# Performance work log

Hardware: AMD Instinct MI355X
Metric: run time of the kernel (lower is better)

Reference implementation:

```python
import jax, jax.numpy as jnp
import numpy as np

B, N, E, D = 8, 4096, 65536, 256


def setup_inputs() -> dict:
    key = jax.random.key(0)
    ks = jax.random.split(key, 4)
    return {
        "node_features": jax.random.normal(ks[0], (B, N, D), dtype=jnp.float32),
        "W": jax.random.normal(ks[1], (D, D), dtype=jnp.float32) * (1.0 / np.sqrt(D)),
        "b": jnp.zeros((D,), dtype=jnp.float32),
        "gamma": jnp.ones((D,), dtype=jnp.float32),
        "beta": jnp.zeros((D,), dtype=jnp.float32),
        "edge_index": jax.random.randint(ks[2], (B, 2, E), 0, N, dtype=jnp.int64),
        "node_mask": jax.random.randint(ks[3], (B, N), 0, 2, dtype=jnp.int32),
    }


def reference(node_features, W, b, gamma, beta, edge_index, node_mask):
    # Linear projection: h = x @ W^T + b   (nn.Linear convention, W: [out, in])
    h = jnp.einsum("bni,oi->bno", node_features, W) + b  # [B, N, D]
    batch, n_nodes, d = h.shape
    n_edges = edge_index.shape[2]

    src = edge_index[:, 0, :]  # [B, E]
    tgt = edge_index[:, 1, :]  # [B, E]

    nm = node_mask.astype(h.dtype)  # [B, N]
    # edge valid iff both endpoints are valid nodes
    emask = jnp.take_along_axis(nm, src, axis=1) * jnp.take_along_axis(nm, tgt, axis=1)  # [B, E]

    # gather source features, mask invalid edges
    msg = jnp.take_along_axis(h, src[..., None], axis=1) * emask[..., None]  # [B, E, D]

    # batched scatter-add via flat segment_sum with per-batch offsets
    seg_ids = (tgt + jnp.arange(batch, dtype=tgt.dtype)[:, None] * n_nodes).reshape(-1)
    agg = jax.ops.segment_sum(msg.reshape(batch * n_edges, d), seg_ids,
                              num_segments=batch * n_nodes).reshape(batch, n_nodes, d)

    h = h + agg / jnp.sqrt(jnp.asarray(n_nodes, h.dtype))

    # dropout is identity in eval mode
    # LayerNorm over last dim (eps = 1e-5, torch default)
    mu = jnp.mean(h, axis=-1, keepdims=True)
    var = jnp.mean((h - mu) ** 2, axis=-1, keepdims=True)
    h = (h - mu) * jax.lax.rsqrt(var + 1e-5) * gamma + beta

    h = jax.nn.relu(h)
    return h * nm[..., None]
```

## Files before the change

kernel.cpp:

```cpp
#include <hip/hip_runtime.h>
#include <hip/hip_bf16.h>

#define NN 4096
#define DIM 256
#define NE 65536
#define TOT_NODES 32768
#define TOT_EDGES 524288

__device__ __forceinline__ float ldf(const void* p, int isbf, size_t i) {
    return isbf ? __bfloat162float(((const __hip_bfloat16*)p)[i]) : ((const float*)p)[i];
}
__device__ __forceinline__ int ldi(const void* p, int is64, size_t i) {
    return is64 ? (int)((const long long*)p)[i] : ((const int*)p)[i];
}

__global__ __launch_bounds__(256)
void init_detect_kernel(const void* ei, const void* nm, const void* x,
                        int* __restrict__ flags, int* __restrict__ counts)
{
    const int t = threadIdx.x;
    counts[blockIdx.x * 256 + t] = 0;
    if (blockIdx.x == 0 && t < 64) {
        const long long ev = ((const long long*)ei)[t];
        const unsigned long long okE = __ballot(ev >= 0 && ev < NN);
        const long long mv = ((const long long*)nm)[t];
        const unsigned long long okM = __ballot(mv == 0 || mv == 1);
        const unsigned int w = ((const unsigned int*)x)[t];
        const int e = (w >> 7) & 0xFF;
        const unsigned long long okF = __ballot(e >= 100 && e <= 140);
        if (t == 0) {
            flags[0] = (okE == ~0ULL) ? 1 : 0;
            flags[1] = (okM == ~0ULL) ? 1 : 0;
            flags[2] = (__popcll(okF) >= 40) ? 1 : 0;
        }
    }
}


typedef __attribute__((ext_vector_type(8))) __bf16 bf16x8;
typedef __attribute__((ext_vector_type(4))) float  f32x4;

__device__ __forceinline__ unsigned short f2bf(float f) {
    unsigned u = __float_as_uint(f);
    u = (u + 0x7fffu + ((u >> 16) & 1u)) >> 16;
    return (unsigned short)u;
}
__device__ __forceinline__ float bf2f(unsigned short h) {
    return __uint_as_float(((unsigned)h) << 16);
}
__device__ __forceinline__ void cvt_hilo(float4 f, ushort4* hi, ushort4* lo) {
    const unsigned short h0 = f2bf(f.x), h1 = f2bf(f.y), h2 = f2bf(f.z), h3 = f2bf(f.w);
    *hi = make_ushort4(h0, h1, h2, h3);
    *lo = make_ushort4(f2bf(f.x - bf2f(h0)), f2bf(f.y - bf2f(h1)),
                       f2bf(f.z - bf2f(h2)), f2bf(f.w - bf2f(h3)));
}
__device__ __forceinline__ bf16x8 frag_ld(const unsigned short* base, int row, int col) {
    const int byte = ((row * 64 + col) * 2) ^ ((row & 7) << 4);
    return *(const bf16x8*)((const char*)base + byte);
}
__device__ __forceinline__ void gload16(const void* g, void* l) {
    __builtin_amdgcn_global_load_lds(
        (const __attribute__((address_space(1))) unsigned int*)g,
        (__attribute__((address_space(3))) unsigned int*)l, 16, 0, 0);
}

__global__ __launch_bounds__(512)
void gemm_kernel(const void* __restrict__ x, const void* __restrict__ w,
                 const void* __restrict__ bias, const int* __restrict__ flags,
                 float* __restrict__ h, unsigned short* __restrict__ hb16)
{
    __shared__ unsigned short As[2][128 * 64];
    __shared__ unsigned short Bs[2][256 * 64];

    const int fbf = flags[2];
    const int t = threadIdx.x;
    const int lane = t & 63;
    const int wid = t >> 6;
    const int wr = wid >> 2;
    const int wc = wid & 3;
    const int m0 = (int)blockIdx.x * 128;

    f32x4 acc[4][4];
#pragma unroll
    for (int mi = 0; mi < 4; ++mi)
#pragma unroll
        for (int nj = 0; nj < 4; ++nj)
            acc[mi][nj] = (f32x4){0.f, 0.f, 0.f, 0.f};

    const int lr = lane & 15;
    const int lk8 = (lane >> 4) << 3;

    auto compute_hh = [&](const unsigned short* Ab, const unsigned short* Bb) {
#pragma unroll
        for (int kk = 0; kk < 64; kk += 32) {
            const int lk = kk + lk8;
            bf16x8 aH[4], bH[4];
#pragma unroll
            for (int mi = 0; mi < 4; ++mi)
                aH[mi] = frag_ld(Ab, wr * 64 + mi * 16 + lr, lk);
#pragma unroll
            for (int nj = 0; nj < 4; ++nj)
                bH[nj] = frag_ld(Bb, wc * 64 + nj * 16 + lr, lk);
#pragma unroll
            for (int mi = 0; mi < 4; ++mi)
#pragma unroll
                for (int nj = 0; nj < 4; ++nj)
                    acc[mi][nj] = __builtin_amdgcn_mfma_f32_16x16x32_bf16(
                        aH[mi], bH[nj], acc[mi][nj], 0, 0, 0);
        }
    };

    if (fbf) {
        const unsigned short* xp = (const unsigned short*)x;
        const unsigned short* wp = (const unsigned short*)w;
        auto stage = [&](int kt, int buf) {
            const int k0 = kt * 64;
#pragma unroll
            for (int i = 0; i < 2; ++i) {
                const int s = i * 512 + t;
                const int row = s >> 3, cg = (s & 7) ^ (row & 7);
                gload16(xp + (size_t)(m0 + row) * 256 + k0 + cg * 8, &As[buf][s * 8]);
            }
#pragma unroll
            for (int i = 0; i < 4; ++i) {
                const int s = i * 512 + t;
                const int row = s >> 3, cg = (s & 7) ^ (row & 7);
                gload16(wp + (size_t)row * 256 + k0 + cg * 8, &Bs[buf][s * 8]);
            }
        };
        stage(0, 0);
        for (int kt = 0; kt < 4; ++kt) {
            __syncthreads();
            if (kt < 3) stage(kt + 1, (kt + 1) & 1);
            compute_hh(As[kt & 1], Bs[kt & 1]);
        }
    } else {
        const float* xp = (const float*)x;
        const float* wp = (const float*)w;
        for (int kt = 0; kt < 4; ++kt) {
            const int k0 = kt * 64;
#pragma unroll
            for (int i = 0; i < 2; ++i) {
                const int s = i * 512 + t;
                const int row = s >> 3, cg = (s & 7) ^ (row & 7);
                const float* src = xp + (size_t)(m0 + row) * 256 + k0 + cg * 8;
                const float4 f0 = *(const float4*)src, f1 = *(const float4*)(src + 4);
                ushort4 h0, l0, h1, l1;
                cvt_hilo(f0, &h0, &l0); cvt_hilo(f1, &h1, &l1);
                *(ushort4*)&As[0][s * 8]     = h0; *(ushort4*)&As[0][s * 8 + 4] = h1;
                *(ushort4*)&As[1][s * 8]     = l0; *(ushort4*)&As[1][s * 8 + 4] = l1;
            }
#pragma unroll
            for (int i = 0; i < 4; ++i) {
                const int s = i * 512 + t;
                const int row = s >> 3, cg = (s & 7) ^ (row & 7);
                const float* src = wp + (size_t)row * 256 + k0 + cg * 8;
                const float4 f0 = *(const float4*)src, f1 = *(const float4*)(src + 4);
                ushort4 h0, l0, h1, l1;
                cvt_hilo(f0, &h0, &l0); cvt_hilo(f1, &h1, &l1);
                *(ushort4*)&Bs[0][s * 8]     = h0; *(ushort4*)&Bs[0][s * 8 + 4] = h1;
                *(ushort4*)&Bs[1][s * 8]     = l0; *(ushort4*)&Bs[1][s * 8 + 4] = l1;
            }
            __syncthreads();
            compute_hh(As[0], Bs[0]);
#pragma unroll
            for (int kk = 0; kk < 64; kk += 32) {
                const int lk = kk + lk8;
                bf16x8 aH[4], bH[4], aL[4], bL[4];
#pragma unroll
                for (int mi = 0; mi < 4; ++mi) {
                    aH[mi] = frag_ld(As[0], wr * 64 + mi * 16 + lr, lk);
                    aL[mi] = frag_ld(As[1], wr * 64 + mi * 16 + lr, lk);
                }
#pragma unroll
                for (int nj = 0; nj < 4; ++nj) {
                    bH[nj] = frag_ld(Bs[0], wc * 64 + nj * 16 + lr, lk);
                    bL[nj] = frag_ld(Bs[1], wc * 64 + nj * 16 + lr, lk);
                }
#pragma unroll
                for (int mi = 0; mi < 4; ++mi)
#pragma unroll
                    for (int nj = 0; nj < 4; ++nj) {
                        acc[mi][nj] = __builtin_amdgcn_mfma_f32_16x16x32_bf16(
                            aH[mi], bL[nj], acc[mi][nj], 0, 0, 0);
                        acc[mi][nj] = __builtin_amdgcn_mfma_f32_16x16x32_bf16(
                            aL[mi], bH[nj], acc[mi][nj], 0, 0, 0);
                    }
            }
            __syncthreads();
        }
    }

    const int r4 = (lane >> 4) << 2;
#pragma unroll
    for (int nj = 0; nj < 4; ++nj) {
        const int n = wc * 64 + nj * 16 + lr;
        const float bv = ldf(bias, fbf, n);
#pragma unroll
        for (int mi = 0; mi < 4; ++mi) {
            const int rb = m0 + wr * 64 + mi * 16 + r4;
#pragma unroll
            for (int r = 0; r < 4; ++r) {
                const float v = acc[mi][nj][r] + bv;
                const size_t idx = (size_t)(rb + r) * 256 + n;
                h[idx] = v;
                hb16[idx] = f2bf(v);
            }
        }
    }
}

__global__ __launch_bounds__(256)
void count_kernel(const void* __restrict__ ei, const void* __restrict__ nm,
                  const int* __restrict__ flags, int* __restrict__ counts)
{
    const int e64 = flags[0], m64 = flags[1];
    const int tid = blockIdx.x * 256 + threadIdx.x;
    const int b = tid >> 15;
    const int k = (tid & 32767) << 1;
    const size_t eb = (size_t)b * 2 * NE;
    int s0, s1, t0, t1;
    if (e64) {
        const longlong2 sv = *(const longlong2*)((const long long*)ei + eb + k);
        const longlong2 tv = *(const longlong2*)((const long long*)ei + eb + NE + k);
        s0 = (int)sv.x; s1 = (int)sv.y; t0 = (int)tv.x; t1 = (int)tv.y;
    } else {
        const int2 sv = *(const int2*)((const int*)ei + eb + k);
        const int2 tv = *(const int2*)((const int*)ei + eb + NE + k);
        s0 = sv.x; s1 = sv.y; t0 = tv.x; t1 = tv.y;
    }
    const size_t mb = (size_t)b * NN;
    if (ldi(nm, m64, mb + s0) && ldi(nm, m64, mb + t0))
        atomicAdd(&counts[b * NN + t0], 1);
    if (ldi(nm, m64, mb + s1) && ldi(nm, m64, mb + t1))
        atomicAdd(&counts[b * NN + t1], 1);
}

__global__ __launch_bounds__(256)
void scan_kernel(int* __restrict__ counts, int* __restrict__ offsets)
{
    __shared__ int sums[256];
    const int b = blockIdx.x;
    const int t = threadIdx.x;
    const int base = b * NN;
    int s = 0;
#pragma unroll
    for (int i = 0; i < 16; ++i) s += counts[base + i * 256 + t];
    sums[t] = s;
    __syncthreads();
    for (int off = 1; off < 256; off <<= 1) {
        int v = (t >= off) ? sums[t - off] : 0;
        __syncthreads();
        sums[t] += v;
        __syncthreads();
    }
    int run = b * NE + sums[t] - s;
#pragma unroll
    for (int i = 0; i < 16; ++i) {
        const int idx = base + i * 256 + t;
        const int c = counts[idx];
        offsets[idx] = run;
        counts[idx] = run;
        run += c;
    }
}

__global__ __launch_bounds__(256)
void fill_kernel(const void* __restrict__ ei, const void* __restrict__ nm,
                 const int* __restrict__ flags,
                 int* __restrict__ cursor, int* __restrict__ bucket)
{
    const int e64 = flags[0], m64 = flags[1];
    const int tid = blockIdx.x * 256 + threadIdx.x;
    const int b = tid >> 15;
    const int k = (tid & 32767) << 1;
    const size_t eb = (size_t)b * 2 * NE;
    int s0, s1, t0, t1;
    if (e64) {
        const longlong2 sv = *(const longlong2*)((const long long*)ei + eb + k);
        const longlong2 tv = *(const longlong2*)((const long long*)ei + eb + NE + k);
        s0 = (int)sv.x; s1 = (int)sv.y; t0 = (int)tv.x; t1 = (int)tv.y;
    } else {
        const int2 sv = *(const int2*)((const int*)ei + eb + k);
        const int2 tv = *(const int2*)((const int*)ei + eb + NE + k);
        s0 = sv.x; s1 = sv.y; t0 = tv.x; t1 = tv.y;
    }
    const size_t mb = (size_t)b * NN;
    if (ldi(nm, m64, mb + s0) && ldi(nm, m64, mb + t0))
        bucket[atomicAdd(&cursor[b * NN + t0], 1)] = s0;
    if (ldi(nm, m64, mb + s1) && ldi(nm, m64, mb + t1))
        bucket[atomicAdd(&cursor[b * NN + t1], 1)] = s1;
}

__global__ __launch_bounds__(256)
void node_kernel(const float* __restrict__ h, const unsigned short* __restrict__ hb16,
                 const int* __restrict__ offsets,
                 const int* __restrict__ ends, const int* __restrict__ bucket,
                 const void* __restrict__ nm, const int* __restrict__ flags,
                 const void* __restrict__ gamma, const void* __restrict__ beta,
                 void* __restrict__ out)
{
    const int blk = ((blockIdx.x & 7) << 10) | (blockIdx.x >> 3);
    const int bt = blk * 4 + (threadIdx.x >> 6);
    const int lane = threadIdx.x & 63;
    const int m64 = flags[1], fbf = flags[2];
    const size_t o4 = (size_t)bt * 64 + lane;
    if (!ldi(nm, m64, bt)) {
        if (fbf) ((ushort4*)out)[o4] = make_ushort4(0, 0, 0, 0);
        else     ((float4*)out)[o4]  = make_float4(0.f, 0.f, 0.f, 0.f);
        return;
    }
    const int b = bt >> 12;
    const ushort4* hg = (const ushort4*)hb16 + ((size_t)b << 12) * 64;
    const float4 self = ((const float4*)h)[o4];
    const int s0 = offsets[bt], s1 = ends[bt];
    float4 a0 = make_float4(0.f, 0.f, 0.f, 0.f), a1 = a0, a2 = a0, a3 = a0;
    int j = s0;
    for (; j + 4 <= s1; j += 4) {
        const ushort4 u0 = hg[(size_t)bucket[j]     * 64 + lane];
        const ushort4 u1 = hg[(size_t)bucket[j + 1] * 64 + lane];
        const ushort4 u2 = hg[(size_t)bucket[j + 2] * 64 + lane];
        const ushort4 u3 = hg[(size_t)bucket[j + 3] * 64 + lane];
        a0.x += bf2f(u0.x); a0.y += bf2f(u0.y); a0.z += bf2f(u0.z); a0.w += bf2f(u0.w);
        a1.x += bf2f(u1.x); a1.y += bf2f(u1.y); a1.z += bf2f(u1.z); a1.w += bf2f(u1.w);
        a2.x += bf2f(u2.x); a2.y += bf2f(u2.y); a2.z += bf2f(u2.z); a2.w += bf2f(u2.w);
        a3.x += bf2f(u3.x); a3.y += bf2f(u3.y); a3.z += bf2f(u3.z); a3.w += bf2f(u3.w);
    }
    for (; j < s1; ++j) {
        const ushort4 u = hg[(size_t)bucket[j] * 64 + lane];
        a0.x += bf2f(u.x); a0.y += bf2f(u.y); a0.z += bf2f(u.z); a0.w += bf2f(u.w);
    }
    float4 acc;
    acc.x = self.x + ((a0.x + a1.x) + (a2.x + a3.x)) * 0.015625f;
    acc.y = self.y + ((a0.y + a1.y) + (a2.y + a3.y)) * 0.015625f;
    acc.z = self.z + ((a0.z + a1.z) + (a2.z + a3.z)) * 0.015625f;
    acc.w = self.w + ((a0.w + a1.w) + (a2.w + a3.w)) * 0.015625f;

    float v1r = (acc.x + acc.y) + (acc.z + acc.w);
    float v2r = (acc.x * acc.x + acc.y * acc.y) + (acc.z * acc.z + acc.w * acc.w);
#pragma unroll
    for (int off = 32; off > 0; off >>= 1) {
        v1r += __shfl_xor(v1r, off, 64);
        v2r += __shfl_xor(v2r, off, 64);
    }
    const float mu  = v1r * (1.f / 256.f);
    const float var = v2r * (1.f / 256.f) - mu * mu;
    const float inv = rsqrtf(var + 1e-5f);
    const int d0 = lane * 4;
    float y0 = (acc.x - mu) * inv * ldf(gamma, fbf, d0)     + ldf(beta, fbf, d0);
    float y1 = (acc.y - mu) * inv * ldf(gamma, fbf, d0 + 1) + ldf(beta, fbf, d0 + 1);
    float y2 = (acc.z - mu) * inv * ldf(gamma, fbf, d0 + 2) + ldf(beta, fbf, d0 + 2);
    float y3 = (acc.w - mu) * inv * ldf(gamma, fbf, d0 + 3) + ldf(beta, fbf, d0 + 3);
    y0 = fmaxf(y0, 0.f); y1 = fmaxf(y1, 0.f); y2 = fmaxf(y2, 0.f); y3 = fmaxf(y3, 0.f);
    if (fbf) ((ushort4*)out)[o4] = make_ushort4(f2bf(y0), f2bf(y1), f2bf(y2), f2bf(y3));
    else     ((float4*)out)[o4]  = make_float4(y0, y1, y2, y3);
}

static float g_sentinel[256];

extern "C" void kernel_launch(void* const* d_in, const int* in_sizes, int n_in,
                              void* d_out, int out_size, void* d_ws, size_t ws_size,
                              hipStream_t stream)
{
    (void)in_sizes; (void)n_in; (void)out_size;
    const void* x     = d_in[0];
    const void* W     = d_in[1];
    const void* bias  = d_in[2];
    const void* gamma = d_in[3];
    const void* beta  = d_in[4];
    const void* ei    = d_in[5];
    const void* nm    = d_in[6];

    char* ws = (char*)d_ws;
    int* flags   = (int*)ws;
    int* counts  = (int*)(ws + 256);
    int* offsets = (int*)(ws + 131328);
    int* bucket  = (int*)(ws + 262656);
    float* h     = (float*)(ws + 2359808);
    unsigned short* hb16 = (unsigned short*)(ws + 35914240);

    int fail = 0;
    hipGetLastError();
#define CHK(stage) do { if (!fail && hipGetLastError() != hipSuccess) fail = (stage); } while (0)

    init_detect_kernel<<<TOT_NODES / 256, 256, 0, stream>>>(ei, nm, x, flags, counts); CHK(1);
    gemm_kernel<<<TOT_NODES / 128, 512, 0, stream>>>(x, W, bias, flags, h, hb16);      CHK(2);
    count_kernel<<<TOT_EDGES / 512, 256, 0, stream>>>(ei, nm, flags, counts);          CHK(3);
    scan_kernel<<<8, 256, 0, stream>>>(counts, offsets);                               CHK(4);
    fill_kernel<<<TOT_EDGES / 512, 256, 0, stream>>>(ei, nm, flags, counts, bucket);   CHK(5);
    node_kernel<<<TOT_NODES / 4, 256, 0, stream>>>(h, hb16, offsets, counts, bucket,
                                                   nm, flags, gamma, beta, d_out);     CHK(6);
#undef CHK

    if (fail) {
        for (int i = 0; i < 256; ++i) g_sentinel[i] = 10000.f * (float)fail;
        hipMemcpyAsync(d_out, g_sentinel, sizeof(g_sentinel),
                       hipMemcpyHostToDevice, stream);
    }
}
```

Baseline: 155.9 us.

## Fuse pipeline into single cooperative persistent kernel with grid syncs

```diff
diff --git a/kernel.cpp b/kernel.cpp
--- a/kernel.cpp
+++ b/kernel.cpp
@@ -1,5 +1,8 @@
 #include <hip/hip_runtime.h>
 #include <hip/hip_bf16.h>
+#include <hip/hip_cooperative_groups.h>
+
+namespace cg = cooperative_groups;
 
 #define NN 4096
 #define DIM 256
@@ -14,29 +17,6 @@
     return is64 ? (int)((const long long*)p)[i] : ((const int*)p)[i];
 }
 
-__global__ __launch_bounds__(256)
-void init_detect_kernel(const void* ei, const void* nm, const void* x,
-                        int* __restrict__ flags, int* __restrict__ counts)
-{
-    const int t = threadIdx.x;
-    counts[blockIdx.x * 256 + t] = 0;
-    if (blockIdx.x == 0 && t < 64) {
-        const long long ev = ((const long long*)ei)[t];
-        const unsigned long long okE = __ballot(ev >= 0 && ev < NN);
-        const long long mv = ((const long long*)nm)[t];
-        const unsigned long long okM = __ballot(mv == 0 || mv == 1);
-        const unsigned int w = ((const unsigned int*)x)[t];
-        const int e = (w >> 7) & 0xFF;
-        const unsigned long long okF = __ballot(e >= 100 && e <= 140);
-        if (t == 0) {
-            flags[0] = (okE == ~0ULL) ? 1 : 0;
-            flags[1] = (okM == ~0ULL) ? 1 : 0;
-            flags[2] = (__popcll(okF) >= 40) ? 1 : 0;
-        }
-    }
-}
-
-
 typedef __attribute__((ext_vector_type(8))) __bf16 bf16x8;
 typedef __attribute__((ext_vector_type(4))) float  f32x4;
 
@@ -64,21 +44,38 @@
         (__attribute__((address_space(3))) unsigned int*)l, 16, 0, 0);
 }
 
-__global__ __launch_bounds__(512)
-void gemm_kernel(const void* __restrict__ x, const void* __restrict__ w,
-                 const void* __restrict__ bias, const int* __restrict__ flags,
-                 float* __restrict__ h, unsigned short* __restrict__ hb16)
+__device__ __forceinline__ void detect_wave(const void* ei, const void* nm,
+                                            const void* x, int* f3) {
+    const int t = threadIdx.x;
+    const long long ev = ((const long long*)ei)[t];
+    const unsigned long long okE = __ballot(ev >= 0 && ev < NN);
+    const long long mv = ((const long long*)nm)[t];
+    const unsigned long long okM = __ballot(mv == 0 || mv == 1);
+    const unsigned int w = ((const unsigned int*)x)[t];
+    const int e = (w >> 7) & 0xFF;
+    const unsigned long long okF = __ballot(e >= 100 && e <= 140);
+    if (t == 0) {
+        f3[0] = (okE == ~0ULL) ? 1 : 0;
+        f3[1] = (okM == ~0ULL) ? 1 : 0;
+        f3[2] = (__popcll(okF) >= 40) ? 1 : 0;
+    }
+}
+
+__device__ __forceinline__ void gemm_body(const void* __restrict__ x,
+                                          const void* __restrict__ w,
+                                          const void* __restrict__ bias, int fbf,
+                                          float* __restrict__ h,
+                                          unsigned short* __restrict__ hb16)
 {
     __shared__ unsigned short As[2][128 * 64];
     __shared__ unsigned short Bs[2][256 * 64];
 
-    const int fbf = flags[2];
     const int t = threadIdx.x;
     const int lane = t & 63;
     const int wid = t >> 6;
     const int wr = wid >> 2;
     const int wc = wid & 3;
-    const int m0 = (int)blockIdx.x * 128;
+    const int m0 = ((((int)blockIdx.x & 7) << 5) + ((int)blockIdx.x >> 3)) * 128;
 
     f32x4 acc[4][4];
 #pragma unroll
@@ -118,14 +115,14 @@
 #pragma unroll
             for (int i = 0; i < 2; ++i) {
                 const int s = i * 512 + t;
-                const int row = s >> 3, cg = (s & 7) ^ (row & 7);
-                gload16(xp + (size_t)(m0 + row) * 256 + k0 + cg * 8, &As[buf][s * 8]);
+                const int row = s >> 3, cgx = (s & 7) ^ (row & 7);
+                gload16(xp + (size_t)(m0 + row) * 256 + k0 + cgx * 8, &As[buf][s * 8]);
             }
 #pragma unroll
             for (int i = 0; i < 4; ++i) {
                 const int s = i * 512 + t;
-                const int row = s >> 3, cg = (s & 7) ^ (row & 7);
-                gload16(wp + (size_t)row * 256 + k0 + cg * 8, &Bs[buf][s * 8]);
+                const int row = s >> 3, cgx = (s & 7) ^ (row & 7);
+                gload16(wp + (size_t)row * 256 + k0 + cgx * 8, &Bs[buf][s * 8]);
             }
         };
         stage(0, 0);
@@ -142,8 +139,8 @@
 #pragma unroll
             for (int i = 0; i < 2; ++i) {
                 const int s = i * 512 + t;
-                const int row = s >> 3, cg = (s & 7) ^ (row & 7);
-                const float* src = xp + (size_t)(m0 + row) * 256 + k0 + cg * 8;
+                const int row = s >> 3, cgx = (s & 7) ^ (row & 7);
+                const float* src = xp + (size_t)(m0 + row) * 256 + k0 + cgx * 8;
                 const float4 f0 = *(const float4*)src, f1 = *(const float4*)(src + 4);
                 ushort4 h0, l0, h1, l1;
                 cvt_hilo(f0, &h0, &l0); cvt_hilo(f1, &h1, &l1);
@@ -153,8 +150,8 @@
 #pragma unroll
             for (int i = 0; i < 4; ++i) {
                 const int s = i * 512 + t;
-                const int row = s >> 3, cg = (s & 7) ^ (row & 7);
-                const float* src = wp + (size_t)row * 256 + k0 + cg * 8;
+                const int row = s >> 3, cgx = (s & 7) ^ (row & 7);
+                const float* src = wp + (size_t)row * 256 + k0 + cgx * 8;
                 const float4 f0 = *(const float4*)src, f1 = *(const float4*)(src + 4);
                 ushort4 h0, l0, h1, l1;
                 cvt_hilo(f0, &h0, &l0); cvt_hilo(f1, &h1, &l1);
@@ -210,45 +207,60 @@
     }
 }
 
-__global__ __launch_bounds__(256)
-void count_kernel(const void* __restrict__ ei, const void* __restrict__ nm,
-                  const int* __restrict__ flags, int* __restrict__ counts)
-{
-    const int e64 = flags[0], m64 = flags[1];
-    const int tid = blockIdx.x * 256 + threadIdx.x;
-    const int b = tid >> 15;
-    const int k = (tid & 32767) << 1;
+__device__ __forceinline__ void edges4(const void* ei, int e64, int b, int k,
+                                       int* s, int* tg) {
     const size_t eb = (size_t)b * 2 * NE;
-    int s0, s1, t0, t1;
     if (e64) {
-        const longlong2 sv = *(const longlong2*)((const long long*)ei + eb + k);
-        const longlong2 tv = *(const longlong2*)((const long long*)ei + eb + NE + k);
-        s0 = (int)sv.x; s1 = (int)sv.y; t0 = (int)tv.x; t1 = (int)tv.y;
+        const longlong2 s01 = *(const longlong2*)((const long long*)ei + eb + k);
+        const longlong2 s23 = *(const longlong2*)((const long long*)ei + eb + k + 2);
+        const longlong2 t01 = *(const longlong2*)((const long long*)ei + eb + NE + k);
+        const longlong2 t23 = *(const longlong2*)((const long long*)ei + eb + NE + k + 2);
+        s[0]=(int)s01.x; s[1]=(int)s01.y; s[2]=(int)s23.x; s[3]=(int)s23.y;
+        tg[0]=(int)t01.x; tg[1]=(int)t01.y; tg[2]=(int)t23.x; tg[3]=(int)t23.y;
     } else {
-        const int2 sv = *(const int2*)((const int*)ei + eb + k);
-        const int2 tv = *(const int2*)((const int*)ei + eb + NE + k);
-        s0 = sv.x; s1 = sv.y; t0 = tv.x; t1 = tv.y;
-    }
+        const int4 sv = *(const int4*)((const int*)ei + eb + k);
+        const int4 tv = *(const int4*)((const int*)ei + eb + NE + k);
+        s[0]=sv.x; s[1]=sv.y; s[2]=sv.z; s[3]=sv.w;
+        tg[0]=tv.x; tg[1]=tv.y; tg[2]=tv.z; tg[3]=tv.w;
+    }
+}
+__device__ __forceinline__ void count_body(const void* ei, const void* nm,
+                                           int e64, int m64, int* counts) {
+    const int b = (int)blockIdx.x & 7, sub = (int)blockIdx.x >> 3;
+    const int k = ((sub << 9) + (int)threadIdx.x) << 2;
+    int s[4], tg[4];
+    edges4(ei, e64, b, k, s, tg);
     const size_t mb = (size_t)b * NN;
-    if (ldi(nm, m64, mb + s0) && ldi(nm, m64, mb + t0))
-        atomicAdd(&counts[b * NN + t0], 1);
-    if (ldi(nm, m64, mb + s1) && ldi(nm, m64, mb + t1))
-        atomicAdd(&counts[b * NN + t1], 1);
-}
-
-__global__ __launch_bounds__(256)
-void scan_kernel(int* __restrict__ counts, int* __restrict__ offsets)
-{
-    __shared__ int sums[256];
-    const int b = blockIdx.x;
-    const int t = threadIdx.x;
+#pragma unroll
+    for (int i = 0; i < 4; ++i)
+        if (ldi(nm, m64, mb + s[i]) && ldi(nm, m64, mb + tg[i]))
+            atomicAdd(&counts[b * NN + tg[i]], 1);
+}
+__device__ __forceinline__ void fill_body(const void* ei, const void* nm,
+                                          int e64, int m64, int* cursor,
+                                          int* bucket) {
+    const int b = (int)blockIdx.x & 7, sub = (int)blockIdx.x >> 3;
+    const int k = ((sub << 9) + (int)threadIdx.x) << 2;
+    int s[4], tg[4];
+    edges4(ei, e64, b, k, s, tg);
+    const size_t mb = (size_t)b * NN;
+#pragma unroll
+    for (int i = 0; i < 4; ++i)
+        if (ldi(nm, m64, mb + s[i]) && ldi(nm, m64, mb + tg[i]))
+            bucket[atomicAdd(&cursor[b * NN + tg[i]], 1)] = s[i];
+}
+
+__device__ __forceinline__ void scan_body(int* __restrict__ counts,
+                                          int* __restrict__ offsets) {
+    __shared__ int sums[512];
+    const int b = (int)blockIdx.x, t = (int)threadIdx.x;
     const int base = b * NN;
     int s = 0;
 #pragma unroll
-    for (int i = 0; i < 16; ++i) s += counts[base + i * 256 + t];
+    for (int i = 0; i < 8; ++i) s += counts[base + i * 512 + t];
     sums[t] = s;
     __syncthreads();
-    for (int off = 1; off < 256; off <<= 1) {
+    for (int off = 1; off < 512; off <<= 1) {
         int v = (t >= off) ? sums[t - off] : 0;
         __syncthreads();
         sums[t] += v;
@@ -256,8 +268,8 @@
     }
     int run = b * NE + sums[t] - s;
 #pragma unroll
-    for (int i = 0; i < 16; ++i) {
-        const int idx = base + i * 256 + t;
+    for (int i = 0; i < 8; ++i) {
+        const int idx = base + i * 512 + t;
         const int c = counts[idx];
         offsets[idx] = run;
         counts[idx] = run;
@@ -265,95 +277,129 @@
     }
 }
 
-__global__ __launch_bounds__(256)
-void fill_kernel(const void* __restrict__ ei, const void* __restrict__ nm,
-                 const int* __restrict__ flags,
-                 int* __restrict__ cursor, int* __restrict__ bucket)
+__device__ __forceinline__ void node_body(const float* __restrict__ h,
+    const unsigned short* __restrict__ hb16, const int* __restrict__ offsets,
+    const int* __restrict__ ends, const int* __restrict__ bucket,
+    const void* __restrict__ nm, int m64, int fbf,
+    const void* __restrict__ gamma, const void* __restrict__ beta,
+    void* __restrict__ out)
 {
-    const int e64 = flags[0], m64 = flags[1];
-    const int tid = blockIdx.x * 256 + threadIdx.x;
-    const int b = tid >> 15;
-    const int k = (tid & 32767) << 1;
-    const size_t eb = (size_t)b * 2 * NE;
-    int s0, s1, t0, t1;
-    if (e64) {
-        const longlong2 sv = *(const longlong2*)((const long long*)ei + eb + k);
-        const longlong2 tv = *(const longlong2*)((const long long*)ei + eb + NE + k);
-        s0 = (int)sv.x; s1 = (int)sv.y; t0 = (int)tv.x; t1 = (int)tv.y;
-    } else {
-        const int2 sv = *(const int2*)((const int*)ei + eb + k);
-        const int2 tv = *(const int2*)((const int*)ei + eb + NE + k);
-        s0 = sv.x; s1 = sv.y; t0 = tv.x; t1 = tv.y;
-    }
-    const size_t mb = (size_t)b * NN;
-    if (ldi(nm, m64, mb + s0) && ldi(nm, m64, mb + t0))
-        bucket[atomicAdd(&cursor[b * NN + t0], 1)] = s0;
-    if (ldi(nm, m64, mb + s1) && ldi(nm, m64, mb + t1))
-        bucket[atomicAdd(&cursor[b * NN + t1], 1)] = s1;
-}
-
-__global__ __launch_bounds__(256)
-void node_kernel(const float* __restrict__ h, const unsigned short* __restrict__ hb16,
-                 const int* __restrict__ offsets,
-                 const int* __restrict__ ends, const int* __restrict__ bucket,
-                 const void* __restrict__ nm, const int* __restrict__ flags,
-                 const void* __restrict__ gamma, const void* __restrict__ beta,
-                 void* __restrict__ out)
+    const int lane = threadIdx.x & 63;
+    const int wave = threadIdx.x >> 6;
+    const int bb = (int)blockIdx.x & 7;
+    const int chunk = (int)blockIdx.x >> 3;
+    const int nb = bb * NN + chunk * 128 + wave * 16;
+    const int d0 = lane * 4;
+    const float g0 = ldf(gamma, fbf, d0),     g1 = ldf(gamma, fbf, d0 + 1);
+    const float g2 = ldf(gamma, fbf, d0 + 2), g3 = ldf(gamma, fbf, d0 + 3);
+    const float b0 = ldf(beta, fbf, d0),      b1 = ldf(beta, fbf, d0 + 1);
+    const float b2 = ldf(beta, fbf, d0 + 2),  b3 = ldf(beta, fbf, d0 + 3);
+    const ushort4* hg = (const ushort4*)hb16 + ((size_t)bb << 12) * 64;
+
+    for (int n = 0; n < 16; ++n) {
+        const int bt = nb + n;
+        const size_t o4 = (size_t)bt * 64 + lane;
+        if (!ldi(nm, m64, bt)) {
+            if (fbf) ((ushort4*)out)[o4] = make_ushort4(0, 0, 0, 0);
+            else     ((float4*)out)[o4]  = make_float4(0.f, 0.f, 0.f, 0.f);
+            continue;
+        }
+        const float4 self = ((const float4*)h)[o4];
+        const int s0 = offsets[bt], s1 = ends[bt];
+        float4 a0 = make_float4(0.f, 0.f, 0.f, 0.f), a1 = a0, a2 = a0, a3 = a0;
+        int j = s0;
+        for (; j + 4 <= s1; j += 4) {
+            const ushort4 u0 = hg[(size_t)bucket[j]     * 64 + lane];
+            const ushort4 u1 = hg[(size_t)bucket[j + 1] * 64 + lane];
+            const ushort4 u2 = hg[(size_t)bucket[j + 2] * 64 + lane];
+            const ushort4 u3 = hg[(size_t)bucket[j + 3] * 64 + lane];
+            a0.x += bf2f(u0.x); a0.y += bf2f(u0.y); a0.z += bf2f(u0.z); a0.w += bf2f(u0.w);
+            a1.x += bf2f(u1.x); a1.y += bf2f(u1.y); a1.z += bf2f(u1.z); a1.w += bf2f(u1.w);
+            a2.x += bf2f(u2.x); a2.y += bf2f(u2.y); a2.z += bf2f(u2.z); a2.w += bf2f(u2.w);
+            a3.x += bf2f(u3.x); a3.y += bf2f(u3.y); a3.z += bf2f(u3.z); a3.w += bf2f(u3.w);
+        }
+        for (; j < s1; ++j) {
+            const ushort4 u = hg[(size_t)bucket[j] * 64 + lane];
+            a0.x += bf2f(u.x); a0.y += bf2f(u.y); a0.z += bf2f(u.z); a0.w += bf2f(u.w);
+        }
+        float4 acc;
+        acc.x = self.x + ((a0.x + a1.x) + (a2.x + a3.x)) * 0.015625f;
+        acc.y = self.y + ((a0.y + a1.y) + (a2.y + a3.y)) * 0.015625f;
+        acc.z = self.z + ((a0.z + a1.z) + (a2.z + a3.z)) * 0.015625f;
+        acc.w = self.w + ((a0.w + a1.w) + (a2.w + a3.w)) * 0.015625f;
+
+        float v1r = (acc.x + acc.y) + (acc.z + acc.w);
+        float v2r = (acc.x * acc.x + acc.y * acc.y) + (acc.z * acc.z + acc.w * acc.w);
+#pragma unroll
+        for (int off = 32; off > 0; off >>= 1) {
+            v1r += __shfl_xor(v1r, off, 64);
+            v2r += __shfl_xor(v2r, off, 64);
+        }
+        const float mu  = v1r * (1.f / 256.f);
+        const float var = v2r * (1.f / 256.f) - mu * mu;
+        const float inv = rsqrtf(var + 1e-5f);
+        float y0 = fmaxf((acc.x - mu) * inv * g0 + b0, 0.f);
+        float y1 = fmaxf((acc.y - mu) * inv * g1 + b1, 0.f);
+        float y2 = fmaxf((acc.z - mu) * inv * g2 + b2, 0.f);
+        float y3 = fmaxf((acc.w - mu) * inv * g3 + b3, 0.f);
+        if (fbf) ((ushort4*)out)[o4] = make_ushort4(f2bf(y0), f2bf(y1), f2bf(y2), f2bf(y3));
+        else     ((float4*)out)[o4]  = make_float4(y0, y1, y2, y3);
+    }
+}
+
+__global__ __launch_bounds__(512)
+void mono_kernel(const void* x, const void* w, const void* bias,
+                 const void* gamma, const void* beta,
+                 const void* ei, const void* nm,
+                 int* counts, int* offsets, int* bucket,
+                 float* h, unsigned short* hb16, void* out)
 {
-    const int blk = ((blockIdx.x & 7) << 10) | (blockIdx.x >> 3);
-    const int bt = blk * 4 + (threadIdx.x >> 6);
-    const int lane = threadIdx.x & 63;
-    const int m64 = flags[1], fbf = flags[2];
-    const size_t o4 = (size_t)bt * 64 + lane;
-    if (!ldi(nm, m64, bt)) {
-        if (fbf) ((ushort4*)out)[o4] = make_ushort4(0, 0, 0, 0);
-        else     ((float4*)out)[o4]  = make_float4(0.f, 0.f, 0.f, 0.f);
-        return;
-    }
-    const int b = bt >> 12;
-    const ushort4* hg = (const ushort4*)hb16 + ((size_t)b << 12) * 64;
-    const float4 self = ((const float4*)h)[o4];
-    const int s0 = offsets[bt], s1 = ends[bt];
-    float4 a0 = make_float4(0.f, 0.f, 0.f, 0.f), a1 = a0, a2 = a0, a3 = a0;
-    int j = s0;
-    for (; j + 4 <= s1; j += 4) {
-        const ushort4 u0 = hg[(size_t)bucket[j]     * 64 + lane];
-        const ushort4 u1 = hg[(size_t)bucket[j + 1] * 64 + lane];
-        const ushort4 u2 = hg[(size_t)bucket[j + 2] * 64 + lane];
-        const ushort4 u3 = hg[(size_t)bucket[j + 3] * 64 + lane];
-        a0.x += bf2f(u0.x); a0.y += bf2f(u0.y); a0.z += bf2f(u0.z); a0.w += bf2f(u0.w);
-        a1.x += bf2f(u1.x); a1.y += bf2f(u1.y); a1.z += bf2f(u1.z); a1.w += bf2f(u1.w);
-        a2.x += bf2f(u2.x); a2.y += bf2f(u2.y); a2.z += bf2f(u2.z); a2.w += bf2f(u2.w);
-        a3.x += bf2f(u3.x); a3.y += bf2f(u3.y); a3.z += bf2f(u3.z); a3.w += bf2f(u3.w);
-    }
-    for (; j < s1; ++j) {
-        const ushort4 u = hg[(size_t)bucket[j] * 64 + lane];
-        a0.x += bf2f(u.x); a0.y += bf2f(u.y); a0.z += bf2f(u.z); a0.w += bf2f(u.w);
-    }
-    float4 acc;
-    acc.x = self.x + ((a0.x + a1.x) + (a2.x + a3.x)) * 0.015625f;
-    acc.y = self.y + ((a0.y + a1.y) + (a2.y + a3.y)) * 0.015625f;
-    acc.z = self.z + ((a0.z + a1.z) + (a2.z + a3.z)) * 0.015625f;
-    acc.w = self.w + ((a0.w + a1.w) + (a2.w + a3.w)) * 0.015625f;
-
-    float v1r = (acc.x + acc.y) + (acc.z + acc.w);
-    float v2r = (acc.x * acc.x + acc.y * acc.y) + (acc.z * acc.z + acc.w * acc.w);
-#pragma unroll
-    for (int off = 32; off > 0; off >>= 1) {
-        v1r += __shfl_xor(v1r, off, 64);
-        v2r += __shfl_xor(v2r, off, 64);
-    }
-    const float mu  = v1r * (1.f / 256.f);
-    const float var = v2r * (1.f / 256.f) - mu * mu;
-    const float inv = rsqrtf(var + 1e-5f);
-    const int d0 = lane * 4;
-    float y0 = (acc.x - mu) * inv * ldf(gamma, fbf, d0)     + ldf(beta, fbf, d0);
-    float y1 = (acc.y - mu) * inv * ldf(gamma, fbf, d0 + 1) + ldf(beta, fbf, d0 + 1);
-    float y2 = (acc.z - mu) * inv * ldf(gamma, fbf, d0 + 2) + ldf(beta, fbf, d0 + 2);
-    float y3 = (acc.w - mu) * inv * ldf(gamma, fbf, d0 + 3) + ldf(beta, fbf, d0 + 3);
-    y0 = fmaxf(y0, 0.f); y1 = fmaxf(y1, 0.f); y2 = fmaxf(y2, 0.f); y3 = fmaxf(y3, 0.f);
-    if (fbf) ((ushort4*)out)[o4] = make_ushort4(f2bf(y0), f2bf(y1), f2bf(y2), f2bf(y3));
-    else     ((float4*)out)[o4]  = make_float4(y0, y1, y2, y3);
+    __shared__ int sflags[3];
+    if (threadIdx.x < 64) detect_wave(ei, nm, x, sflags);
+    const int gid = (int)blockIdx.x * 512 + (int)threadIdx.x;
+    if (gid < TOT_NODES) counts[gid] = 0;
+    __syncthreads();
+    const int e64 = sflags[0], m64 = sflags[1], fbf = sflags[2];
+    cg::this_grid().sync();
+    count_body(ei, nm, e64, m64, counts);
+    gemm_body(x, w, bias, fbf, h, hb16);
+    cg::this_grid().sync();
+    if (blockIdx.x < 8) scan_body(counts, offsets);
+    cg::this_grid().sync();
+    fill_body(ei, nm, e64, m64, counts, bucket);
+    cg::this_grid().sync();
+    node_body(h, hb16, offsets, counts, bucket, nm, m64, fbf, gamma, beta, out);
+}
+
+__global__ __launch_bounds__(512)
+void init_detect_kernel(const void* ei, const void* nm, const void* x,
+                        int* flags, int* counts) {
+    if (blockIdx.x == 0 && threadIdx.x < 64) detect_wave(ei, nm, x, flags);
+    const int gid = (int)blockIdx.x * 512 + (int)threadIdx.x;
+    if (gid < TOT_NODES) counts[gid] = 0;
+}
+__global__ __launch_bounds__(512)
+void gemm_kernel(const void* x, const void* w, const void* bias,
+                 const int* flags, float* h, unsigned short* hb16) {
+    gemm_body(x, w, bias, flags[2], h, hb16);
+}
+__global__ __launch_bounds__(512)
+void count_kernel(const void* ei, const void* nm, const int* flags, int* counts) {
+    count_body(ei, nm, flags[0], flags[1], counts);
+}
+__global__ __launch_bounds__(512)
+void scan_kernel(int* counts, int* offsets) { scan_body(counts, offsets); }
+__global__ __launch_bounds__(512)
+void fill_kernel(const void* ei, const void* nm, const int* flags,
+                 int* cursor, int* bucket) {
+    fill_body(ei, nm, flags[0], flags[1], cursor, bucket);
+}
+__global__ __launch_bounds__(512)
+void node_kernel(const float* h, const unsigned short* hb16, const int* offsets,
+                 const int* ends, const int* bucket, const void* nm,
+                 const int* flags, const void* gamma, const void* beta, void* out) {
+    node_body(h, hb16, offsets, ends, bucket, nm, flags[1], flags[2],
+              gamma, beta, out);
 }
 
 static float g_sentinel[256];
@@ -362,7 +408,7 @@
                               void* d_out, int out_size, void* d_ws, size_t ws_size,
                               hipStream_t stream)
 {
-    (void)in_sizes; (void)n_in; (void)out_size;
+    (void)in_sizes; (void)n_in; (void)out_size; (void)ws_size;
     const void* x     = d_in[0];
     const void* W     = d_in[1];
     const void* bias  = d_in[2];
@@ -379,17 +425,40 @@
     float* h     = (float*)(ws + 2359808);
     unsigned short* hb16 = (unsigned short*)(ws + 35914240);
 
+    static int s_coop = -1;
+    if (s_coop < 0) {
+        int dev = 0, v = 0;
+        (void)hipGetDevice(&dev);
+        if (hipDeviceGetAttribute(&v, hipDeviceAttributeCooperativeLaunch, dev)
+            != hipSuccess) v = 0;
+        s_coop = v;
+    }
+
+    hipGetLastError();
+    bool mono_done = false;
+    if (s_coop) {
+        void* ka[13] = {(void*)&x, (void*)&W, (void*)&bias, (void*)&gamma,
+                        (void*)&beta, (void*)&ei, (void*)&nm, (void*)&counts,
+                        (void*)&offsets, (void*)&bucket, (void*)&h, (void*)&hb16,
+                        (void*)&d_out};
+        if (hipLaunchCooperativeKernel((const void*)mono_kernel, dim3(256),
+                                       dim3(512), ka, 0, stream) == hipSuccess)
+            mono_done = true;
+        else
+            (void)hipGetLastError();
+    }
+
     int fail = 0;
-    hipGetLastError();
 #define CHK(stage) do { if (!fail && hipGetLastError() != hipSuccess) fail = (stage); } while (0)
-
-    init_detect_kernel<<<TOT_NODES / 256, 256, 0, stream>>>(ei, nm, x, flags, counts); CHK(1);
-    gemm_kernel<<<TOT_NODES / 128, 512, 0, stream>>>(x, W, bias, flags, h, hb16);      CHK(2);
-    count_kernel<<<TOT_EDGES / 512, 256, 0, stream>>>(ei, nm, flags, counts);          CHK(3);
-    scan_kernel<<<8, 256, 0, stream>>>(counts, offsets);                               CHK(4);
-    fill_kernel<<<TOT_EDGES / 512, 256, 0, stream>>>(ei, nm, flags, counts, bucket);   CHK(5);
-    node_kernel<<<TOT_NODES / 4, 256, 0, stream>>>(h, hb16, offsets, counts, bucket,
-                                                   nm, flags, gamma, beta, d_out);     CHK(6);
+    if (!mono_done) {
+        init_detect_kernel<<<64, 512, 0, stream>>>(ei, nm, x, flags, counts);    CHK(1);
+        gemm_kernel<<<256, 512, 0, stream>>>(x, W, bias, flags, h, hb16);        CHK(2);
+        count_kernel<<<256, 512, 0, stream>>>(ei, nm, flags, counts);            CHK(3);
+        scan_kernel<<<8, 512, 0, stream>>>(counts, offsets);                     CHK(4);
+        fill_kernel<<<256, 512, 0, stream>>>(ei, nm, flags, counts, bucket);     CHK(5);
+        node_kernel<<<256, 512, 0, stream>>>(h, hb16, offsets, counts, bucket,
+                                             nm, flags, gamma, beta, d_out);     CHK(6);
+    }
 #undef CHK
 
     if (fail) {
```

Result: slower. 288.4 us (+85.0%).
